# Kernel optimization log

Measured on AMD Instinct MI355X. Metric: run time of the kernel, lower is better.

## Reference

```python
import jax, jax.numpy as jnp
import numpy as np

THR = 1.0                      # spike threshold
DECAY_V = float(np.exp(-1.0 / 20.0))
GAMMA = 0.3                    # surrogate-gradient dampening factor
OUT_DECAY = 0.8                # exp_convolve decay

@jax.custom_vjp
def spike_fn(v_scaled):
    # Heaviside spike with pseudo-derivative gamma*max(0, 1-|v_scaled|)
    return (v_scaled > 0.0).astype(v_scaled.dtype)

def _spike_fwd(v_scaled):
    return spike_fn(v_scaled), v_scaled

def _spike_bwd(v_scaled, g):
    return (g * GAMMA * jnp.maximum(0.0, 1.0 - jnp.abs(v_scaled)),)

spike_fn.defvjp(_spike_fwd, _spike_bwd)


def setup_inputs() -> dict:
    key = jax.random.key(0)
    k1, k2, k3, k4 = jax.random.split(key, 4)
    B, T, NI, NR = 32, 1000, 128, 512
    inputs = jax.random.normal(k1, (B, T, NI), dtype=jnp.float32)
    w_in = jax.random.normal(k2, (NI, NR), dtype=jnp.float32) / np.sqrt(NI)
    w_rec = jax.random.normal(k3, (NR, NR), dtype=jnp.float32) / np.sqrt(NR)
    w_out = jax.random.normal(k4, (NR, 1), dtype=jnp.float32) / np.sqrt(NR)
    b_out = jnp.zeros((1,), dtype=jnp.float32)
    return {"inputs": inputs, "w_in": w_in, "w_rec": w_rec, "w_out": w_out, "b_out": b_out}


def reference(inputs, w_in, w_rec, w_out, b_out):
    B, T, _ = inputs.shape
    NR = w_rec.shape[0]
    dtype = inputs.dtype
    # no autapses (zero diagonal on recurrent weights, as in LSNN cells)
    w_rec_masked = w_rec * (1.0 - jnp.eye(NR, dtype=dtype))
    # precompute feedforward input currents: [T, B, NR]
    i_in = jnp.swapaxes(jnp.einsum('bti,iu->btu', inputs, w_in), 0, 1)

    def lif_step(carry, x_t):
        v, z = carry
        i_t = x_t + z @ w_rec_masked           # [B, NR]
        v_new = DECAY_V * v + i_t - z * THR    # reset by subtraction
        z_new = spike_fn((v_new - THR) / THR)
        return (v_new, z_new), (v_new, z_new)

    v0 = jnp.zeros((B, NR), dtype)
    z0 = jnp.zeros((B, NR), dtype)
    _, (vs, zs) = jax.lax.scan(lif_step, (v0, z0), i_in)
    voltages = jnp.swapaxes(vs, 0, 1)  # [B, T, NR]
    spikes = jnp.swapaxes(zs, 0, 1)    # [B, T, NR]

    proj = spikes @ w_out + b_out      # [B, T, 1]

    def filt_step(a, x):
        a_new = OUT_DECAY * a + (1.0 - OUT_DECAY) * x
        return a_new, a_new

    f0 = jnp.zeros((B, 1), dtype)
    _, pred = jax.lax.scan(filt_step, f0, jnp.swapaxes(proj, 0, 1))
    prediction = jnp.swapaxes(pred, 0, 1)  # [B, T, 1]
    return voltages, spikes, prediction
```

## Files before the change

kernel.cpp:

```cpp
#include <hip/hip_runtime.h>

#define NR 512
#define NI 128
#define B 32
#define T 1000
#define G 16
#define LA (256 + G)

__device__ __forceinline__ float mul_nofma(float a, float b) {
    float r = a * b;
    asm volatile("" : "+v"(r));
    return r;
}

__global__ __launch_bounds__(512) void k_prep(const float* __restrict__ w_rec,
                                              float* __restrict__ w_ws) {
    const int r = blockIdx.x, u = threadIdx.x;
    float val = 0.f;
    if (r < NR && r != u) val = w_rec[r * NR + u];
    w_ws[r * NR + u] = val;
}

template <int ROWS>
__global__ __launch_bounds__(512) void k_in_gemm(const float* __restrict__ inputs,
                                                 const float* __restrict__ w_in,
                                                 float* __restrict__ i_in) {
    const int u = threadIdx.x;
    const int r0 = blockIdx.x * ROWS;
    float acc[ROWS];
#pragma unroll
    for (int r = 0; r < ROWS; ++r) acc[r] = 0.f;
    const float* __restrict__ inp = inputs + (long)r0 * NI;
#pragma unroll 4
    for (int i = 0; i < NI; ++i) {
        float w = w_in[i * NR + u];
#pragma unroll
        for (int r = 0; r < ROWS; ++r)
            acc[r] = __builtin_fmaf(inp[r * NI + i], w, acc[r]);
    }
#pragma unroll
    for (int r = 0; r < ROWS; ++r)
        i_in[(long)(r0 + r) * NR + u] = acc[r];
}

__device__ __forceinline__ void loadg(float (&buf)[G], int g, int nlo,
                                      const int* __restrict__ listA,
                                      const int* __restrict__ listB,
                                      const float* __restrict__ w_ws, int u) {
    const int* lp = (g < nlo) ? (listA + g * G) : (listB + (g - nlo) * G);
#pragma unroll
    for (int qq = 0; qq < G / 4; ++qq) {
        int4 jv = *(const int4*)(lp + qq * 4);
        int j0 = __builtin_amdgcn_readfirstlane(jv.x);
        int j1 = __builtin_amdgcn_readfirstlane(jv.y);
        int j2 = __builtin_amdgcn_readfirstlane(jv.z);
        int j3 = __builtin_amdgcn_readfirstlane(jv.w);
        buf[qq * 4 + 0] = w_ws[j0 * NR + u];
        buf[qq * 4 + 1] = w_ws[j1 * NR + u];
        buf[qq * 4 + 2] = w_ws[j2 * NR + u];
        buf[qq * 4 + 3] = w_ws[j3 * NR + u];
    }
}

__device__ __forceinline__ void sumg(const float (&buf)[G], int g, int nlo,
                                     float& s1, float& s2) {
    float& s = (g < nlo) ? s1 : s2;
#pragma unroll
    for (int q = 0; q < G; ++q) s = __fadd_rn(s, buf[q]);
}

__global__ __launch_bounds__(512) void k_scan(const float* __restrict__ w_ws,
                                              const float* __restrict__ w_out,
                                              const float* __restrict__ b_out,
                                              float* __restrict__ out) {
    const int b = blockIdx.x;
    const int u = threadIdx.x;
    const int wav = u >> 6, lane = u & 63;

    float* __restrict__ volt_b = out + (long)b * (T * NR);
    float* __restrict__ spk_b  = out + (long)B * T * NR + (long)b * (T * NR);
    float* __restrict__ pred   = out + 2L * B * T * NR + (long)b * T;

    __shared__ __align__(16) int listA[LA];
    __shared__ __align__(16) int listB[LA];
    __shared__ int wcnt[8];
    __shared__ double projp[8];

    if (u >= 256 && u < 256 + G) { listA[u] = NR; listB[u] = NR; }

    float v = 0.f, z = 0.f;
    const float decay = 0.951229424500714f;
    const double wo = (double)w_out[u];
    const double bo = (double)b_out[0];
    double ema = 0.0;
    __syncthreads();

    for (int t = 0; t < T; ++t) {
        float ii = volt_b[t * NR + u];

        unsigned long long m = __ballot(z > 0.5f);
        double p = (double)z * wo;
#pragma unroll
        for (int o = 32; o > 0; o >>= 1) p += __shfl_xor(p, o, 64);
        if (lane == 0) { wcnt[wav] = __popcll(m); projp[wav] = p; }
        __syncthreads();

        const int c0 = wcnt[0], c1 = wcnt[1], c2 = wcnt[2], c3 = wcnt[3];
        const int c4 = wcnt[4], c5 = wcnt[5], c6 = wcnt[6], c7 = wcnt[7];
        const int cnt_lo = c0 + c1 + c2 + c3;
        const int cnt_hi = c4 + c5 + c6 + c7;

        if (z > 0.5f) {
            int below = __popcll(m & ((1ull << lane) - 1ull));
            if (wav < 4) {
                int pos = (wav > 0 ? c0 : 0) + (wav > 1 ? c1 : 0) + (wav > 2 ? c2 : 0) + below;
                listA[pos] = u;
            } else {
                int pos = (wav > 4 ? c4 : 0) + (wav > 5 ? c5 : 0) + (wav > 6 ? c6 : 0) + below;
                listB[pos] = u;
            }
        }
        if (u < 256) { if (u >= cnt_lo) listA[u] = NR; }
        else         { int x = u - 256; if (x >= cnt_hi) listB[x] = NR; }

        if (u == 0 && t > 0) {
            double pr = bo;
#pragma unroll
            for (int w2 = 0; w2 < 8; ++w2) pr += projp[w2];
            ema = 0.8 * ema + 0.2 * pr;
            pred[t - 1] = (float)ema;
        }
        __syncthreads();

        const int nlo = (cnt_lo + G - 1) >> 4;
        const int ng  = nlo + ((cnt_hi + G - 1) >> 4);
        float s1 = 0.f, s2 = 0.f;
        if (ng > 0) {
            float bA[G], bB[G];
            loadg(bA, 0, nlo, listA, listB, w_ws, u);
            int g = 0;
            while (true) {
                if (g + 1 < ng) loadg(bB, g + 1, nlo, listA, listB, w_ws, u);
                sumg(bA, g, nlo, s1, s2);
                ++g;
                if (g == ng) break;
                if (g + 1 < ng) loadg(bA, g + 1, nlo, listA, listB, w_ws, u);
                sumg(bB, g, nlo, s1, s2);
                ++g;
                if (g == ng) break;
            }
        }
        float rec = __fadd_rn(s1, s2);

        float it = __fadd_rn(ii, rec);
        float m1 = mul_nofma(decay, v);
        float t2 = __fadd_rn(m1, it);
        float vn = __fsub_rn(t2, z);
        float zn = (vn > 1.0f) ? 1.0f : 0.0f;
        volt_b[t * NR + u] = vn;
        spk_b[t * NR + u]  = zn;
        v = vn; z = zn;
    }

    {
        double p = (double)z * wo;
#pragma unroll
        for (int o = 32; o > 0; o >>= 1) p += __shfl_xor(p, o, 64);
        if (lane == 0) projp[wav] = p;
        __syncthreads();
        if (u == 0) {
            double pr = bo;
#pragma unroll
            for (int w2 = 0; w2 < 8; ++w2) pr += projp[w2];
            ema = 0.8 * ema + 0.2 * pr;
            pred[T - 1] = (float)ema;
        }
    }
}

__global__ __launch_bounds__(512) void k_scan_ref(const float* __restrict__ w_rec,
                                                  const float* __restrict__ w_out,
                                                  const float* __restrict__ b_out,
                                                  float* __restrict__ out) {
    const int b = blockIdx.x;
    const int u = threadIdx.x;
    const int wav = u >> 6, lane = u & 63;
    const int KC = 256;

    float* __restrict__ volt_b = out + (long)b * (T * NR);
    float* __restrict__ spk_b  = out + (long)B * T * NR + (long)b * (T * NR);
    float* __restrict__ pred   = out + 2L * B * T * NR;

    __shared__ __align__(16) int list[NR];
    __shared__ int wcnt[8];
    __shared__ double projp[8];

    float v = 0.f, z = 0.f;
    const float decay = 0.951229424500714f;
    const double wo = (double)w_out[u];
    const double bo = (double)b_out[0];
    double ema = 0.0;

    for (int t = 0; t < T; ++t) {
        unsigned long long m = __ballot(z > 0.5f);
        if (lane == 0) wcnt[wav] = __popcll(m);
        __syncthreads();
        int cnt = 0, base = 0;
#pragma unroll
        for (int w2 = 0; w2 < 8; ++w2) {
            int c = wcnt[w2];
            if (w2 < wav) base += c;
            cnt += c;
        }
        if (z > 0.5f) {
            int pos = base + __popcll(m & ((1ull << lane) - 1ull));
            list[pos] = u;
        }
        float ii = volt_b[t * NR + u];
        __syncthreads();

        float s1 = 0.f, s2 = 0.f;
        int k = 0;
        for (; k + 8 <= cnt; k += 8) {
            int4 ja = *(const int4*)&list[k];
            int4 jb = *(const int4*)&list[k + 4];
            int j0 = __builtin_amdgcn_readfirstlane(ja.x);
            int j1 = __builtin_amdgcn_readfirstlane(ja.y);
            int j2 = __builtin_amdgcn_readfirstlane(ja.z);
            int j3 = __builtin_amdgcn_readfirstlane(ja.w);
            int j4 = __builtin_amdgcn_readfirstlane(jb.x);
            int j5 = __builtin_amdgcn_readfirstlane(jb.y);
            int j6 = __builtin_amdgcn_readfirstlane(jb.z);
            int j7 = __builtin_amdgcn_readfirstlane(jb.w);
            float w0 = w_rec[j0 * NR + u]; if (j0 == u) w0 = 0.f;
            float w1 = w_rec[j1 * NR + u]; if (j1 == u) w1 = 0.f;
            float w2 = w_rec[j2 * NR + u]; if (j2 == u) w2 = 0.f;
            float w3 = w_rec[j3 * NR + u]; if (j3 == u) w3 = 0.f;
            float w4 = w_rec[j4 * NR + u]; if (j4 == u) w4 = 0.f;
            float w5 = w_rec[j5 * NR + u]; if (j5 == u) w5 = 0.f;
            float w6 = w_rec[j6 * NR + u]; if (j6 == u) w6 = 0.f;
            float w7 = w_rec[j7 * NR + u]; if (j7 == u) w7 = 0.f;
            if (j0 < KC) s1 = __fadd_rn(s1, w0); else s2 = __fadd_rn(s2, w0);
            if (j1 < KC) s1 = __fadd_rn(s1, w1); else s2 = __fadd_rn(s2, w1);
            if (j2 < KC) s1 = __fadd_rn(s1, w2); else s2 = __fadd_rn(s2, w2);
            if (j3 < KC) s1 = __fadd_rn(s1, w3); else s2 = __fadd_rn(s2, w3);
            if (j4 < KC) s1 = __fadd_rn(s1, w4); else s2 = __fadd_rn(s2, w4);
            if (j5 < KC) s1 = __fadd_rn(s1, w5); else s2 = __fadd_rn(s2, w5);
            if (j6 < KC) s1 = __fadd_rn(s1, w6); else s2 = __fadd_rn(s2, w6);
            if (j7 < KC) s1 = __fadd_rn(s1, w7); else s2 = __fadd_rn(s2, w7);
        }
        for (; k < cnt; ++k) {
            int j = __builtin_amdgcn_readfirstlane(list[k]);
            float w = w_rec[j * NR + u];
            if (j == u) w = 0.f;
            if (j < KC) s1 = __fadd_rn(s1, w); else s2 = __fadd_rn(s2, w);
        }
        float rec = __fadd_rn(s1, s2);

        float it = __fadd_rn(ii, rec);
        float m1 = mul_nofma(decay, v);
        float t2 = __fadd_rn(m1, it);
        float vn = __fsub_rn(t2, z);
        float zn = (vn > 1.0f) ? 1.0f : 0.0f;
        volt_b[t * NR + u] = vn;
        spk_b[t * NR + u]  = zn;

        double p = (double)zn * wo;
#pragma unroll
        for (int o = 32; o > 0; o >>= 1) p += __shfl_xor(p, o, 64);
        if (lane == 0) projp[wav] = p;
        __syncthreads();
        if (u == 0) {
            double pr = bo;
#pragma unroll
            for (int w2 = 0; w2 < 8; ++w2) pr += projp[w2];
            ema = 0.8 * ema + 0.2 * pr;
            pred[b * T + t] = (float)ema;
        }
        v = vn; z = zn;
    }
}

extern "C" void kernel_launch(void* const* d_in, const int* in_sizes, int n_in,
                              void* d_out, int out_size, void* d_ws, size_t ws_size,
                              hipStream_t stream) {
    const float* inputs = (const float*)d_in[0];
    const float* w_in   = (const float*)d_in[1];
    const float* w_rec  = (const float*)d_in[2];
    const float* w_out  = (const float*)d_in[3];
    const float* b_out  = (const float*)d_in[4];
    float* out = (float*)d_out;

    k_in_gemm<16><<<dim3(B * T / 16), dim3(512), 0, stream>>>(inputs, w_in, out);

    const size_t need = (size_t)(NR + 1) * NR * sizeof(float);
    if (ws_size >= need) {
        float* w_ws = (float*)d_ws;
        k_prep<<<dim3(NR + 1), dim3(512), 0, stream>>>(w_rec, w_ws);
        k_scan<<<dim3(B), dim3(512), 0, stream>>>(w_ws, w_out, b_out, out);
    } else {
        k_scan_ref<<<dim3(B), dim3(512), 0, stream>>>(w_rec, w_out, b_out, out);
    }
}
```

Baseline: 2.596 ms.

## Move output projection to separate kernel, deepen weight prefetch, lighten barriers

```diff
diff --git a/kernel.cpp b/kernel.cpp
--- a/kernel.cpp
+++ b/kernel.cpp
@@ -5,12 +5,16 @@
 #define B 32
 #define T 1000
 #define G 16
-#define LA (256 + G)
+#define LB 320
 
 __device__ __forceinline__ float mul_nofma(float a, float b) {
     float r = a * b;
     asm volatile("" : "+v"(r));
     return r;
+}
+
+__device__ __forceinline__ void bar_lds() {
+    asm volatile("s_waitcnt lgkmcnt(0)\n\ts_barrier" ::: "memory");
 }
 
 __global__ __launch_bounds__(512) void k_prep(const float* __restrict__ w_rec,
@@ -70,8 +74,6 @@
 }
 
 __global__ __launch_bounds__(512) void k_scan(const float* __restrict__ w_ws,
-                                              const float* __restrict__ w_out,
-                                              const float* __restrict__ b_out,
                                               float* __restrict__ out) {
     const int b = blockIdx.x;
     const int u = threadIdx.x;
@@ -79,31 +81,23 @@
 
     float* __restrict__ volt_b = out + (long)b * (T * NR);
     float* __restrict__ spk_b  = out + (long)B * T * NR + (long)b * (T * NR);
-    float* __restrict__ pred   = out + 2L * B * T * NR + (long)b * T;
-
-    __shared__ __align__(16) int listA[LA];
-    __shared__ __align__(16) int listB[LA];
+
+    __shared__ __align__(16) int listA[NR / 2];
+    __shared__ __align__(16) int listB[LB];
     __shared__ int wcnt[8];
-    __shared__ double projp[8];
-
-    if (u >= 256 && u < 256 + G) { listA[u] = NR; listB[u] = NR; }
+
+    if (u >= 256 && u < 256 + 64) listB[u] = NR;
 
     float v = 0.f, z = 0.f;
     const float decay = 0.951229424500714f;
-    const double wo = (double)w_out[u];
-    const double bo = (double)b_out[0];
-    double ema = 0.0;
     __syncthreads();
 
     for (int t = 0; t < T; ++t) {
         float ii = volt_b[t * NR + u];
 
         unsigned long long m = __ballot(z > 0.5f);
-        double p = (double)z * wo;
-#pragma unroll
-        for (int o = 32; o > 0; o >>= 1) p += __shfl_xor(p, o, 64);
-        if (lane == 0) { wcnt[wav] = __popcll(m); projp[wav] = p; }
-        __syncthreads();
+        if (lane == 0) wcnt[wav] = __popcll(m);
+        bar_lds();
 
         const int c0 = wcnt[0], c1 = wcnt[1], c2 = wcnt[2], c3 = wcnt[3];
         const int c4 = wcnt[4], c5 = wcnt[5], c6 = wcnt[6], c7 = wcnt[7];
@@ -122,32 +116,26 @@
         }
         if (u < 256) { if (u >= cnt_lo) listA[u] = NR; }
         else         { int x = u - 256; if (x >= cnt_hi) listB[x] = NR; }
-
-        if (u == 0 && t > 0) {
-            double pr = bo;
-#pragma unroll
-            for (int w2 = 0; w2 < 8; ++w2) pr += projp[w2];
-            ema = 0.8 * ema + 0.2 * pr;
-            pred[t - 1] = (float)ema;
-        }
-        __syncthreads();
+        bar_lds();
 
         const int nlo = (cnt_lo + G - 1) >> 4;
         const int ng  = nlo + ((cnt_hi + G - 1) >> 4);
         float s1 = 0.f, s2 = 0.f;
-        if (ng > 0) {
-            float bA[G], bB[G];
-            loadg(bA, 0, nlo, listA, listB, w_ws, u);
+        {
+            float b0[G], b1[G], b2[G], b3[G];
+            loadg(b0, 0, nlo, listA, listB, w_ws, u);
+            loadg(b1, 1, nlo, listA, listB, w_ws, u);
+            loadg(b2, 2, nlo, listA, listB, w_ws, u);
             int g = 0;
-            while (true) {
-                if (g + 1 < ng) loadg(bB, g + 1, nlo, listA, listB, w_ws, u);
-                sumg(bA, g, nlo, s1, s2);
-                ++g;
-                if (g == ng) break;
-                if (g + 1 < ng) loadg(bA, g + 1, nlo, listA, listB, w_ws, u);
-                sumg(bB, g, nlo, s1, s2);
-                ++g;
-                if (g == ng) break;
+            while (g < ng) {
+                loadg(b3, g + 3, nlo, listA, listB, w_ws, u);
+                sumg(b0, g, nlo, s1, s2); ++g; if (g == ng) break;
+                loadg(b0, g + 3, nlo, listA, listB, w_ws, u);
+                sumg(b1, g, nlo, s1, s2); ++g; if (g == ng) break;
+                loadg(b1, g + 3, nlo, listA, listB, w_ws, u);
+                sumg(b2, g, nlo, s1, s2); ++g; if (g == ng) break;
+                loadg(b2, g + 3, nlo, listA, listB, w_ws, u);
+                sumg(b3, g, nlo, s1, s2); ++g;
             }
         }
         float rec = __fadd_rn(s1, s2);
@@ -161,19 +149,39 @@
         spk_b[t * NR + u]  = zn;
         v = vn; z = zn;
     }
-
-    {
-        double p = (double)z * wo;
+}
+
+__global__ __launch_bounds__(512) void k_pred(const float* __restrict__ w_out,
+                                              const float* __restrict__ b_out,
+                                              float* __restrict__ out) {
+    const int b = blockIdx.x;
+    const int tid = threadIdx.x;
+    const int wav = tid >> 6, lane = tid & 63;
+    const float* __restrict__ spk_b = out + (long)B * T * NR + (long)b * (T * NR);
+    float* __restrict__ pred = out + 2L * B * T * NR + (long)b * T;
+
+    __shared__ double projs[T];
+
+    double wo[8];
+#pragma unroll
+    for (int q = 0; q < 8; ++q) wo[q] = (double)w_out[lane + q * 64];
+
+    for (int t = wav; t < T; t += 8) {
+        double p = 0.0;
+#pragma unroll
+        for (int q = 0; q < 8; ++q)
+            p += (double)spk_b[t * NR + lane + q * 64] * wo[q];
 #pragma unroll
         for (int o = 32; o > 0; o >>= 1) p += __shfl_xor(p, o, 64);
-        if (lane == 0) projp[wav] = p;
-        __syncthreads();
-        if (u == 0) {
-            double pr = bo;
-#pragma unroll
-            for (int w2 = 0; w2 < 8; ++w2) pr += projp[w2];
-            ema = 0.8 * ema + 0.2 * pr;
-            pred[T - 1] = (float)ema;
+        if (lane == 0) projs[t] = p;
+    }
+    __syncthreads();
+    if (tid == 0) {
+        const double bo = (double)b_out[0];
+        double ema = 0.0;
+        for (int t = 0; t < T; ++t) {
+            ema = 0.8 * ema + 0.2 * (bo + projs[t]);
+            pred[t] = (float)ema;
         }
     }
 }
@@ -297,7 +305,8 @@
     if (ws_size >= need) {
         float* w_ws = (float*)d_ws;
         k_prep<<<dim3(NR + 1), dim3(512), 0, stream>>>(w_rec, w_ws);
-        k_scan<<<dim3(B), dim3(512), 0, stream>>>(w_ws, w_out, b_out, out);
+        k_scan<<<dim3(B), dim3(512), 0, stream>>>(w_ws, out);
+        k_pred<<<dim3(B), dim3(512), 0, stream>>>(w_out, b_out, out);
     } else {
         k_scan_ref<<<dim3(B), dim3(512), 0, stream>>>(w_rec, w_out, b_out, out);
     }
```

New measurement: 3.217 ms. 1.24x slower.
